# Performance work log

Measured on AMD Instinct MI355X. Metric: run time of the kernel, lower is better.

Reference implementation:

```python
import jax, jax.numpy as jnp
import numpy as np
from jax import lax

B, L, C_IN, D, H = 256, 4096, 2, 128, 4
DH = D // H          # 32 head dim
FF = 192             # round_up(1.3 * 128, 64)
NUM_CLASSES = 5
EPS = 1e-5


def setup_inputs() -> dict:
    key = jax.random.key(0)
    it = iter(jax.random.split(key, 48))
    def r(*s):
        return jax.random.normal(next(it), s, jnp.float32) * 0.1
    return dict(
        x=jax.random.normal(next(it), (B, L, C_IN), jnp.float32),
        w1a=r(16, C_IN, 4), w1b=r(16, C_IN, 2),
        bn1_g=jnp.ones((32,), jnp.float32), bn1_b=jnp.zeros((32,), jnp.float32),
        bn1_m=r(32), bn1_v=jnp.ones((32,), jnp.float32),
        w2=r(64, 32, 3),
        bn2_g=jnp.ones((64,), jnp.float32), bn2_b=jnp.zeros((64,), jnp.float32),
        bn2_m=r(64), bn2_v=jnp.ones((64,), jnp.float32),
        w3=r(D, 64, 3),
        bn3_g=jnp.ones((D,), jnp.float32), bn3_b=jnp.zeros((D,), jnp.float32),
        bn3_m=r(D), bn3_v=jnp.ones((D,), jnp.float32),
        ln1_w=jnp.ones((D,), jnp.float32),
        conv_w=r(D, 1, 3), conv_b=jnp.zeros((D,), jnp.float32),
        wi=r(H, DH, DH), wf=r(H, DH, DH), wz=r(H, DH, DH), wo=r(H, DH, DH),
        rkernel=r(H, DH, 4, DH), rbias=r(4, H, DH),
        gn_w=jnp.ones((D,), jnp.float32),
        ln2_w=jnp.ones((D,), jnp.float32),
        ffn_up_w=r(D, 2 * FF), ffn_down_w=r(FF, D),
        lnp_w=jnp.ones((D,), jnp.float32),
        fc_w=r(D, NUM_CLASSES), fc_b=jnp.zeros((NUM_CLASSES,), jnp.float32),
        lengths=jnp.full((B,), L, jnp.int32),
    )


def _leaky(x):
    return jnp.where(x >= 0, x, 0.01 * x)


def _bn(x, g, b, m, v):  # eval-mode batchnorm, x: (B, C, L)
    return (x - m[:, None]) * (g / jnp.sqrt(v + EPS))[:, None] + b[:, None]


def _conv(x, w, pad, groups=1):  # x: (B, C, L), w: (O, I/groups, K)
    return lax.conv_general_dilated(x, w, (1,), [pad],
                                    dimension_numbers=('NCH', 'OIH', 'NCH'),
                                    feature_group_count=groups)


def _pool(x):  # max pool kernel=2 stride=2 (floor)
    b, c, l = x.shape
    l2 = l // 2
    return x[:, :, :l2 * 2].reshape(b, c, l2, 2).max(-1)


def _ln(x, w):  # LayerNorm, weight only (xlstm lib default bias=False)
    mu = jnp.mean(x, -1, keepdims=True)
    var = jnp.mean((x - mu) ** 2, -1, keepdims=True)
    return (x - mu) * lax.rsqrt(var + EPS) * w


def _forward(x, w1a, w1b, bn1_g, bn1_b, bn1_m, bn1_v, w2, bn2_g, bn2_b, bn2_m, bn2_v,
             w3, bn3_g, bn3_b, bn3_m, bn3_v, ln1_w, conv_w, conv_b, wi, wf, wz, wo,
             rkernel, rbias, gn_w, ln2_w, ffn_up_w, ffn_down_w, lnp_w, fc_w, fc_b, lengths):
    b = x.shape[0]
    # ---- CNN stem (dropout = identity in eval) ----
    xc = jnp.transpose(x, (0, 2, 1))                      # (B, C_in, L)
    h = jnp.concatenate([_conv(xc, w1a, (1, 1)), _conv(xc, w1b, (0, 0))], 1)  # (B, 32, L-1)
    h = _pool(_leaky(_bn(h, bn1_g, bn1_b, bn1_m, bn1_v)))
    h = _pool(_leaky(_bn(_conv(h, w2, (0, 0)), bn2_g, bn2_b, bn2_m, bn2_v)))
    h = _pool(_leaky(_bn(_conv(h, w3, (0, 0)), bn3_g, bn3_b, bn3_m, bn3_v)))
    e = jnp.transpose(h, (0, 2, 1))                       # (B, S, D)
    s = e.shape[1]

    # ---- sLSTM block: pre-LN -> sLSTM layer -> residual ----
    xn = _ln(e, ln1_w)
    # causal depthwise conv (k=3, left pad 2) + SiLU, feeds i/f gates
    xcv = _conv(jnp.transpose(xn, (0, 2, 1)), conv_w, (2, 0), groups=D)
    xcv = jnp.transpose(jax.nn.silu(xcv + conv_b[:, None]), (0, 2, 1))  # (B, S, D)

    def hproj(t, w):  # headwise (block-diagonal) linear
        return jnp.einsum('bshd,hde->bshe', t.reshape(b, s, H, DH), w)

    gx = jnp.stack([hproj(xcv, wi), hproj(xcv, wf), hproj(xn, wz), hproj(xn, wo)], 2)
    gx = jnp.transpose(gx, (1, 0, 2, 3, 4)) + rbias       # (S, B, 4, H, DH)

    def step(carry, g):
        y, c, n, m = carry                                # each (B, H, DH)
        raw = g + jnp.einsum('bhd,hdge->bghe', y, rkernel)  # (B, 4, H, DH)
        iraw, fraw, zraw, oraw = raw[:, 0], raw[:, 1], raw[:, 2], raw[:, 3]
        logfplusm = m + jax.nn.log_sigmoid(fraw)
        mnew = jnp.maximum(iraw, logfplusm)               # stabilizer
        ig = jnp.exp(iraw - mnew)
        fg = jnp.exp(logfplusm - mnew)
        cnew = fg * c + ig * jnp.tanh(zraw)
        nnew = fg * n + ig
        ynew = jax.nn.sigmoid(oraw) * cnew / nnew
        return (ynew, cnew, nnew, mnew), ynew

    z0 = jnp.zeros((b, H, DH), e.dtype)
    _, ys = lax.scan(step, (z0, z0, z0, z0), gx)          # ys: (S, B, H, DH)
    y = jnp.transpose(ys, (1, 0, 2, 3))                   # (B, S, H, DH)
    mu = jnp.mean(y, -1, keepdims=True)
    var = jnp.mean((y - mu) ** 2, -1, keepdims=True)
    y = ((y - mu) * lax.rsqrt(var + EPS)).reshape(b, s, D) * gn_w  # per-head groupnorm
    e = e + y

    # ---- gated GELU feedforward -> residual ----
    xn2 = _ln(e, ln2_w)
    up = xn2 @ ffn_up_w                                   # (B, S, 2*FF)
    e = e + (jax.nn.gelu(up[..., :FF], approximate=False) * up[..., FF:]) @ ffn_down_w

    # ---- post-stack norm, last token, classifier head ----
    e = _ln(e, lnp_w)
    return e[:, -1, :] @ fc_w + fc_b                      # (B, NUM_CLASSES)


def reference(x, w1a, w1b, bn1_g, bn1_b, bn1_m, bn1_v, w2, bn2_g, bn2_b, bn2_m, bn2_v,
              w3, bn3_g, bn3_b, bn3_m, bn3_v, ln1_w, conv_w, conv_b, wi, wf, wz, wo,
              rkernel, rbias, gn_w, ln2_w, ffn_up_w, ffn_down_w, lnp_w, fc_w, fc_b, lengths):
    return _forward(x, w1a, w1b, bn1_g, bn1_b, bn1_m, bn1_v, w2, bn2_g, bn2_b, bn2_m, bn2_v,
                    w3, bn3_g, bn3_b, bn3_m, bn3_v, ln1_w, conv_w, conv_b, wi, wf, wz, wo,
                    rkernel, rbias, gn_w, ln2_w, ffn_up_w, ffn_down_w, lnp_w, fc_w, fc_b, lengths)
```

## Files before the change

kernel.cpp:

```cpp
#include <hip/hip_runtime.h>
#include <hip/hip_bf16.h>
#include <math.h>

#define EPS 1e-5f

typedef __attribute__((ext_vector_type(8))) _Float16 half8;
typedef __attribute__((ext_vector_type(4))) float f32x4;

static __device__ __forceinline__ unsigned short f16u(float x) {
  _Float16 h = (_Float16)x;
  return *(unsigned short*)&h;
}
static __device__ __forceinline__ float uf16(unsigned short u) {
  _Float16 h = *(_Float16*)&u;
  return (float)h;
}

__global__ __launch_bounds__(256) void kWTB2(const float* __restrict__ w2,
    const float* __restrict__ w3, unsigned short* __restrict__ o2,
    unsigned short* __restrict__ o3) {
  int idx = blockIdx.x * 256 + threadIdx.x;
  if (idx < 64 * 104) {
    int oc = idx / 104, kp = idx % 104;
    float v = 0.f;
    if (kp < 96) { int k = kp >> 5, ci = kp & 31; v = w2[oc * 96 + ci * 3 + k]; }
    o2[idx] = f16u(v);
  } else {
    int j = idx - 64 * 104;
    if (j < 128 * 200) {
      int oc = j / 200, kp = j % 200;
      float v = 0.f;
      if (kp < 192) { int k = kp >> 6, ci = kp & 63; v = w3[oc * 192 + ci * 3 + k]; }
      o3[j] = f16u(v);
    }
  }
}

__global__ __launch_bounds__(512) void kConv12(const float* __restrict__ x,
    const float* __restrict__ w1a, const float* __restrict__ w1b,
    const float* __restrict__ g1, const float* __restrict__ b1,
    const float* __restrict__ m1, const float* __restrict__ v1,
    const unsigned short* __restrict__ Bw, const float* __restrict__ g2,
    const float* __restrict__ b2, const float* __restrict__ m2,
    const float* __restrict__ v2, unsigned short* __restrict__ out2) {
  __shared__ _Float16 sA[130 * 40];
  __shared__ _Float16 sB[64 * 104];
  int tid = threadIdx.x;
  int b = blockIdx.z;
  int p0 = blockIdx.x * 128;
  {
    const unsigned int* src = (const unsigned int*)Bw;
    unsigned int* dst = (unsigned int*)sB;
    for (int i = tid; i < 64 * 104 / 2; i += 512) dst[i] = src[i];
  }
  {
    int c = tid & 31, rg = tid >> 5;
    float sc1 = g1[c] * rsqrtf(v1[c] + EPS);
    float sh1 = b1[c] - m1[c] * sc1;
    float wk0[4], wk1[4];
    if (c < 16) {
#pragma unroll
      for (int k = 0; k < 4; k++) { wk0[k] = w1a[c * 8 + k]; wk1[k] = w1a[c * 8 + 4 + k]; }
    } else {
      int cc = c - 16;
#pragma unroll
      for (int k = 0; k < 2; k++) { wk0[k] = w1b[cc * 4 + k]; wk1[k] = w1b[cc * 4 + 2 + k]; }
      wk0[2] = wk0[3] = wk1[2] = wk1[3] = 0.f;
    }
    const float2* xp = (const float2*)(x + (size_t)b * 8192);
    for (int r = rg; r < 130; r += 16) {
      int rr = p0 + r;
      _Float16 outv = (_Float16)0.f;
      if (rr < 2047) {
        float xv0[5], xv1[5];
#pragma unroll
        for (int j = 0; j < 5; j++) {
          int l = 2 * rr - 1 + j;
          if (l >= 0 && l < 4096) { float2 v = xp[l]; xv0[j] = v.x; xv1[j] = v.y; }
          else { xv0[j] = 0.f; xv1[j] = 0.f; }
        }
        float a0 = 0.f, a1 = 0.f;
        if (c < 16) {
#pragma unroll
          for (int k = 0; k < 4; k++) {
            a0 += xv0[k] * wk0[k] + xv1[k] * wk1[k];
            a1 += xv0[k + 1] * wk0[k] + xv1[k + 1] * wk1[k];
          }
        } else {
#pragma unroll
          for (int k = 0; k < 2; k++) {
            a0 += xv0[k + 1] * wk0[k] + xv1[k + 1] * wk1[k];
            a1 += xv0[k + 2] * wk0[k] + xv1[k + 2] * wk1[k];
          }
        }
        a0 = a0 * sc1 + sh1; a1 = a1 * sc1 + sh1;
        a0 = a0 >= 0.f ? a0 : 0.01f * a0;
        a1 = a1 >= 0.f ? a1 : 0.01f * a1;
        outv = (_Float16)fmaxf(a0, a1);
      }
      sA[r * 40 + c] = outv;
    }
  }
  __syncthreads();
  int lane = tid & 63, w = tid >> 6;
  int nrow = lane & 15, quad = lane >> 4;
  f32x4 acc[4];
#pragma unroll
  for (int i = 0; i < 4; i++) acc[i] = (f32x4){0.f, 0.f, 0.f, 0.f};
  int mbase = w * 16;
#pragma unroll
  for (int kk = 0; kk < 3; kk++) {
    half8 a = *(const half8*)(sA + (mbase + nrow + kk) * 40 + quad * 8);
#pragma unroll
    for (int ot = 0; ot < 4; ot++) {
      half8 bb = *(const half8*)(sB + (ot * 16 + nrow) * 104 + kk * 32 + quad * 8);
      acc[ot] = __builtin_amdgcn_mfma_f32_16x16x32_f16(a, bb, acc[ot], 0, 0, 0);
    }
  }
  int gm0 = p0 + mbase + quad * 4;
#pragma unroll
  for (int ot = 0; ot < 4; ot++) {
    int oc = ot * 16 + nrow;
    float sc = g2[oc] * rsqrtf(v2[oc] + EPS);
    float sh = b2[oc] - m2[oc] * sc;
    float v0 = acc[ot][0] * sc + sh, vv1 = acc[ot][1] * sc + sh;
    float v2e = acc[ot][2] * sc + sh, v3 = acc[ot][3] * sc + sh;
    v0 = v0 >= 0.f ? v0 : 0.01f * v0;
    vv1 = vv1 >= 0.f ? vv1 : 0.01f * vv1;
    v2e = v2e >= 0.f ? v2e : 0.01f * v2e;
    v3 = v3 >= 0.f ? v3 : 0.01f * v3;
    float pA = fmaxf(v0, vv1), pB = fmaxf(v2e, v3);
    int t0 = gm0 >> 1, t1 = t0 + 1;
    if (t0 < 1022) out2[((size_t)b * 1022 + t0) * 64 + oc] = f16u(pA);
    if (t1 < 1022) out2[((size_t)b * 1022 + t1) * 64 + oc] = f16u(pB);
  }
}

__global__ __launch_bounds__(512) void kConv3LN(const unsigned short* __restrict__ in,
    const unsigned short* __restrict__ Bw, const float* __restrict__ g,
    const float* __restrict__ bta, const float* __restrict__ mn,
    const float* __restrict__ vr, const float* __restrict__ lnw,
    unsigned short* __restrict__ xn, float* __restrict__ elast) {
  constexpr int IC = 64, OC = 128, LIN = 1022, AP = 72, BP = 200, KSTEPS = 6, OCT = 8;
  __shared__ _Float16 sA[130 * AP];
  __shared__ _Float16 sB[OC * BP];
  int tid = threadIdx.x;
  int b = blockIdx.z;
  int p0 = blockIdx.x * 128;
  {
    const unsigned int* src = (const unsigned int*)Bw;
    unsigned int* dst = (unsigned int*)sB;
    for (int i = tid; i < OC * BP / 2; i += 512) dst[i] = src[i];
  }
  {
    int q = tid % 8;
    for (int r = tid / 8; r < 130; r += 64) {
      int gp = p0 + r;
      uint4 val = {0u, 0u, 0u, 0u};
      if (gp < LIN) val = *(const uint4*)(in + ((size_t)b * LIN + gp) * IC + q * 8);
      *(uint4*)(sA + r * AP + q * 8) = val;
    }
  }
  __syncthreads();
  int lane = tid & 63, w = tid >> 6;
  int nrow = lane & 15, quad = lane >> 4;
  f32x4 acc[OCT];
#pragma unroll
  for (int i = 0; i < OCT; i++) acc[i] = (f32x4){0.f, 0.f, 0.f, 0.f};
  int mbase = w * 16;
#pragma unroll
  for (int kk = 0; kk < KSTEPS; kk++) {
    int k = kk >> 1;
    int ci0 = (kk & 1) * 32;
    half8 a = *(const half8*)(sA + (mbase + nrow + k) * AP + ci0 + quad * 8);
#pragma unroll
    for (int ot = 0; ot < OCT; ot++) {
      half8 bb = *(const half8*)(sB + (ot * 16 + nrow) * BP + kk * 32 + quad * 8);
      acc[ot] = __builtin_amdgcn_mfma_f32_16x16x32_f16(a, bb, acc[ot], 0, 0, 0);
    }
  }
  float pA[OCT], pB[OCT];
  float sA1 = 0.f, sA2 = 0.f, sB1 = 0.f, sB2 = 0.f;
#pragma unroll
  for (int ot = 0; ot < OCT; ot++) {
    int oc = ot * 16 + nrow;
    float sc = g[oc] * rsqrtf(vr[oc] + EPS);
    float sh = bta[oc] - mn[oc] * sc;
    float v0 = acc[ot][0] * sc + sh, v1 = acc[ot][1] * sc + sh;
    float v2 = acc[ot][2] * sc + sh, v3 = acc[ot][3] * sc + sh;
    v0 = v0 >= 0.f ? v0 : 0.01f * v0;
    v1 = v1 >= 0.f ? v1 : 0.01f * v1;
    v2 = v2 >= 0.f ? v2 : 0.01f * v2;
    v3 = v3 >= 0.f ? v3 : 0.01f * v3;
    float a = fmaxf(v0, v1), bb2 = fmaxf(v2, v3);
    pA[ot] = a; pB[ot] = bb2;
    sA1 += a; sA2 += a * a; sB1 += bb2; sB2 += bb2 * bb2;
  }
#pragma unroll
  for (int m = 1; m <= 8; m <<= 1) {
    sA1 += __shfl_xor(sA1, m); sA2 += __shfl_xor(sA2, m);
    sB1 += __shfl_xor(sB1, m); sB2 += __shfl_xor(sB2, m);
  }
  float muA = sA1 * (1.f / 128.f);
  float rsA = rsqrtf(sA2 * (1.f / 128.f) - muA * muA + EPS);
  float muB = sB1 * (1.f / 128.f);
  float rsB = rsqrtf(sB2 * (1.f / 128.f) - muB * muB + EPS);
  int t0 = (p0 + mbase + quad * 4) >> 1, t1 = t0 + 1;
#pragma unroll
  for (int ot = 0; ot < OCT; ot++) {
    int oc = ot * 16 + nrow;
    float lw = lnw[oc];
    if (t0 < 510) xn[((size_t)b * 510 + t0) * OC + oc] = f16u((pA[ot] - muA) * rsA * lw);
    if (t1 < 510) xn[((size_t)b * 510 + t1) * OC + oc] = f16u((pB[ot] - muB) * rsB * lw);
    if (t1 == 509) elast[b * 128 + oc] = pB[ot];
  }
}

__global__ __launch_bounds__(256) void kGxM(const unsigned short* __restrict__ xn,
    const float* __restrict__ cw, const float* __restrict__ cb,
    const float* __restrict__ wi, const float* __restrict__ wf,
    const float* __restrict__ wz, const float* __restrict__ wo,
    const float* __restrict__ rb, unsigned int* __restrict__ gx) {
  __shared__ __align__(16) char smem[29200];
  float* xnf = (float*)smem;
  _Float16* aX = (_Float16*)(smem + 8720);
  _Float16* aN = (_Float16*)(smem + 13840);
  unsigned short* ct = (unsigned short*)smem;
  _Float16* sW = (_Float16*)(smem + 18960);
  int bh = blockIdx.x, b = bh >> 2, h = bh & 3;
  int tid = threadIdx.x, lane = tid & 63, w = tid >> 6;
  int nrow = lane & 15, quad = lane >> 4;
  for (int idx = tid; idx < 4096; idx += 256) {
    int slot = idx >> 11, n = (idx >> 5) & 63, d = idx & 31;
    const float* wp = slot ? ((n >= 32) ? wo : wz) : ((n >= 32) ? wf : wi);
    sW[slot * 2560 + n * 40 + d] = (_Float16)wp[h * 1024 + d * 32 + (n & 31)];
  }
  int dd = tid & 31;
  float cw0 = cw[(h * 32 + dd) * 3], cw1 = cw[(h * 32 + dd) * 3 + 1],
        cw2 = cw[(h * 32 + dd) * 3 + 2], cbv = cb[h * 32 + dd];
  float bias0[4], bias1[4];
#pragma unroll
  for (int nt = 0; nt < 4; nt++) {
    int n = nt * 16 + nrow;
    bias0[nt] = rb[(n >> 5) * 128 + h * 32 + (n & 31)];
    bias1[nt] = rb[(2 + (n >> 5)) * 128 + h * 32 + (n & 31)];
  }
  __syncthreads();
  half8 bw0[4], bw1[4];
#pragma unroll
  for (int nt = 0; nt < 4; nt++) {
    bw0[nt] = *(const half8*)(sW + (nt * 16 + nrow) * 40 + quad * 8);
    bw1[nt] = *(const half8*)(sW + 2560 + (nt * 16 + nrow) * 40 + quad * 8);
  }
  const unsigned short* xb = xn + ((size_t)b * 510) * 128 + h * 32;
  for (int s0 = 0; s0 < 510; s0 += 64) {
    __syncthreads();
    {
      int d2 = tid & 15;
      for (int r = tid >> 4; r < 66; r += 16) {
        int s = s0 - 2 + r;
        unsigned int v = 0;
        if (s >= 0 && s < 510) v = *(const unsigned int*)(xb + (size_t)s * 128 + d2 * 2);
        xnf[r * 33 + d2 * 2]     = uf16(v & 0xFFFFu);
        xnf[r * 33 + d2 * 2 + 1] = uf16(v >> 16);
      }
    }
    __syncthreads();
    for (int m = tid >> 5; m < 64; m += 8) {
      float x0 = xnf[m * 33 + dd], x1 = xnf[(m + 1) * 33 + dd], x2 = xnf[(m + 2) * 33 + dd];
      float a = cbv + cw0 * x0 + cw1 * x1 + cw2 * x2;
      a = a * __builtin_amdgcn_rcpf(1.f + __expf(-a));
      aX[m * 40 + dd] = (_Float16)a;
      aN[m * 40 + dd] = (_Float16)x2;
    }
    __syncthreads();
    f32x4 z = (f32x4){0.f, 0.f, 0.f, 0.f};
    half8 ax = *(const half8*)(aX + (w * 16 + nrow) * 40 + quad * 8);
    half8 an = *(const half8*)(aN + (w * 16 + nrow) * 40 + quad * 8);
    f32x4 acc0[4], acc1[4];
#pragma unroll
    for (int nt = 0; nt < 4; nt++) {
      acc0[nt] = __builtin_amdgcn_mfma_f32_16x16x32_f16(ax, bw0[nt], z, 0, 0, 0);
      acc1[nt] = __builtin_amdgcn_mfma_f32_16x16x32_f16(an, bw1[nt], z, 0, 0, 0);
    }
    __syncthreads();
#pragma unroll
    for (int nt = 0; nt < 4; nt++) {
#pragma unroll
      for (int r = 0; r < 4; r++) {
        int row = w * 16 + quad * 4 + r;
        ct[row * 132 + 2 * (nt * 16 + nrow)]     = f16u(acc0[nt][r] + bias0[nt]);
        ct[row * 132 + 2 * (nt * 16 + nrow) + 1] = f16u(acc1[nt][r] + bias1[nt]);
      }
    }
    __syncthreads();
    {
      int u = tid & 63;
      for (int m = tid >> 6; m < 64; m += 4) {
        int s = s0 + m;
        if (s < 510)
          gx[((size_t)s * 1024 + bh) * 64 + u] = *(const unsigned int*)(ct + m * 132 + 2 * u);
      }
    }
  }
}

__global__ __launch_bounds__(64) void kRec(const unsigned int* __restrict__ gx,
    const float* __restrict__ rk, float* __restrict__ yf) {
  int bh = blockIdx.x; int h = bh & 3;
  int l = threadIdx.x; int half = l >> 5; int e = l & 31;
  float R1[32], R2[32];
  int g1 = half, g2 = 2 + half;
  const float* r1p = rk + h * 4096 + g1 * 32 + e;
  const float* r2p = rk + h * 4096 + g2 * 32 + e;
#pragma unroll
  for (int d = 0; d < 32; d++) { R1[d] = r1p[d * 128]; R2[d] = r2p[d * 128]; }
  const unsigned int* gp = gx + (size_t)bh * 64 + l;
  unsigned int buf[8];
#pragma unroll
  for (int j = 0; j < 8; j++) buf[j] = gp[(size_t)j * 65536];
  float y = 0.f, cst = 0.f, nst = 0.f, mst = 0.f;

  auto step = [&](unsigned int pc) {
    float a1 = uf16(pc & 0xFFFFu);
    float a2 = uf16(pc >> 16);
    float s10 = 0.f, s11 = 0.f, s12 = 0.f, s13 = 0.f;
    float s20 = 0.f, s21 = 0.f, s22 = 0.f, s23 = 0.f;
    unsigned int yb = __float_as_uint(y);
#pragma unroll
    for (int d = 0; d < 32; d += 4) {
      float y0 = __uint_as_float(__builtin_amdgcn_readlane(yb, d));
      float y1 = __uint_as_float(__builtin_amdgcn_readlane(yb, d + 1));
      float y2 = __uint_as_float(__builtin_amdgcn_readlane(yb, d + 2));
      float y3 = __uint_as_float(__builtin_amdgcn_readlane(yb, d + 3));
      s10 = fmaf(y0, R1[d], s10);     s20 = fmaf(y0, R2[d], s20);
      s11 = fmaf(y1, R1[d + 1], s11); s21 = fmaf(y1, R2[d + 1], s21);
      s12 = fmaf(y2, R1[d + 2], s12); s22 = fmaf(y2, R2[d + 2], s22);
      s13 = fmaf(y3, R1[d + 3], s13); s23 = fmaf(y3, R2[d + 3], s23);
    }
    a1 += (s10 + s11) + (s12 + s13);
    a2 += (s20 + s21) + (s22 + s23);
    float en = __expf(-fabsf(a1));
    float ls = fminf(a1, 0.f) - __logf(1.f + en);
    float sg = __builtin_amdgcn_rcpf(1.f + __expf(-a2));
    float tz = 1.f - 2.f * __builtin_amdgcn_rcpf(__expf(2.f * a2) + 1.f);
    float lsf = __shfl_xor(ls, 32);
    float so  = __shfl_xor(sg, 32);
    float lf = mst + lsf;
    float mnew = fmaxf(a1, lf);
    float ig = __expf(a1 - mnew);
    float fg = __expf(lf - mnew);
    cst = fg * cst + ig * tz;
    nst = fg * nst + ig;
    mst = mnew;
    y = so * cst * __builtin_amdgcn_rcpf(nst);
  };

  for (int s0 = 0; s0 < 504; s0 += 8) {
#pragma unroll
    for (int j = 0; j < 8; j++) {
      unsigned int pc = buf[j];
      int sn = s0 + j + 8; sn = sn > 509 ? 509 : sn;
      buf[j] = gp[(size_t)sn * 65536];
      step(pc);
    }
  }
#pragma unroll
  for (int j = 0; j < 6; j++) step(buf[j]);

  if (half == 0) yf[(bh >> 2) * 128 + h * 32 + e] = y;
}

__global__ __launch_bounds__(128) void kHead(const float* __restrict__ yf,
    const float* __restrict__ elast, const float* __restrict__ gnw,
    const float* __restrict__ ln2w, const float* __restrict__ upw,
    const float* __restrict__ dnw, const float* __restrict__ lnpw,
    const float* __restrict__ fcw, const float* __restrict__ fcb,
    float* __restrict__ outp) {
  int c = threadIdx.x; int b = blockIdx.x;
  __shared__ float sred[4];
  __shared__ float sx[128];
  __shared__ float sup[384];
  __shared__ float shh[192];
  float yv = yf[b * 128 + c];
  float s1 = yv, s2 = yv * yv;
#pragma unroll
  for (int m = 1; m <= 16; m <<= 1) { s1 += __shfl_xor(s1, m); s2 += __shfl_xor(s2, m); }
  float mu = s1 * (1.f / 32.f);
  float var = s2 * (1.f / 32.f) - mu * mu;
  float yn = (yv - mu) * rsqrtf(var + EPS) * gnw[c];
  float el = elast[b * 128 + c] + yn;
  auto ln128 = [&](float v, const float* w) -> float {
    float a = v, a2 = v * v;
#pragma unroll
    for (int m = 1; m <= 32; m <<= 1) { a += __shfl_xor(a, m); a2 += __shfl_xor(a2, m); }
    int wv = c >> 6;
    if ((c & 63) == 0) { sred[wv * 2] = a; sred[wv * 2 + 1] = a2; }
    __syncthreads();
    float t1 = sred[0] + sred[2], t2 = sred[1] + sred[3];
    __syncthreads();
    float mm = t1 * (1.f / 128.f);
    float vv = t2 * (1.f / 128.f) - mm * mm;
    return (v - mm) * rsqrtf(vv + EPS) * w[c];
  };
  float xn2 = ln128(el, ln2w);
  sx[c] = xn2;
  __syncthreads();
#pragma unroll
  for (int jj = 0; jj < 3; jj++) {
    int j = c + jj * 128;
    float acc = 0.f;
    for (int k = 0; k < 128; k++) acc += sx[k] * upw[k * 384 + j];
    sup[j] = acc;
  }
  __syncthreads();
  {
    float u = sup[c]; float mg = sup[192 + c];
    shh[c] = 0.5f * u * (1.f + erff(u * 0.70710678118654752f)) * mg;
    if (c < 64) {
      float u2 = sup[128 + c]; float m2 = sup[320 + c];
      shh[128 + c] = 0.5f * u2 * (1.f + erff(u2 * 0.70710678118654752f)) * m2;
    }
  }
  __syncthreads();
  float acc = 0.f;
  for (int f = 0; f < 192; f++) acc += shh[f] * dnw[f * 128 + c];
  float e2 = el + acc;
  float e3 = ln128(e2, lnpw);
  sx[c] = e3;
  __syncthreads();
  if (c < 5) {
    float a = fcb[c];
    for (int k = 0; k < 128; k++) a += sx[k] * fcw[k * 5 + c];
    outp[b * 5 + c] = a;
  }
}

extern "C" void kernel_launch(void* const* d_in, const int* in_sizes, int n_in,
                              void* d_out, int out_size, void* d_ws, size_t ws_size,
                              hipStream_t stream) {
  const float* x    = (const float*)d_in[0];
  const float* w1a  = (const float*)d_in[1];
  const float* w1b  = (const float*)d_in[2];
  const float* bn1g = (const float*)d_in[3];
  const float* bn1b = (const float*)d_in[4];
  const float* bn1m = (const float*)d_in[5];
  const float* bn1v = (const float*)d_in[6];
  const float* w2   = (const float*)d_in[7];
  const float* bn2g = (const float*)d_in[8];
  const float* bn2b = (const float*)d_in[9];
  const float* bn2m = (const float*)d_in[10];
  const float* bn2v = (const float*)d_in[11];
  const float* w3   = (const float*)d_in[12];
  const float* bn3g = (const float*)d_in[13];
  const float* bn3b = (const float*)d_in[14];
  const float* bn3m = (const float*)d_in[15];
  const float* bn3v = (const float*)d_in[16];
  const float* ln1w = (const float*)d_in[17];
  const float* cw   = (const float*)d_in[18];
  const float* cb   = (const float*)d_in[19];
  const float* wi   = (const float*)d_in[20];
  const float* wf   = (const float*)d_in[21];
  const float* wz   = (const float*)d_in[22];
  const float* wo   = (const float*)d_in[23];
  const float* rk   = (const float*)d_in[24];
  const float* rb   = (const float*)d_in[25];
  const float* gnw  = (const float*)d_in[26];
  const float* ln2w = (const float*)d_in[27];
  const float* upw  = (const float*)d_in[28];
  const float* dnw  = (const float*)d_in[29];
  const float* lnpw = (const float*)d_in[30];
  const float* fcw  = (const float*)d_in[31];
  const float* fcb  = (const float*)d_in[32];
  float* outp = (float*)d_out;

  char* ws = (char*)d_ws;
  unsigned short* xnb  = (unsigned short*)ws;
  unsigned short* out2 = (unsigned short*)(ws + ((size_t)34 << 20));
  unsigned int*   gxu  = (unsigned int*)(ws + ((size_t)34 << 20));
  float* elast = (float*)(ws + ((size_t)162 << 20));
  float* yfin  = (float*)(ws + ((size_t)163 << 20));
  unsigned short* wtg2 = (unsigned short*)(ws + ((size_t)164 << 20));
  unsigned short* wtg3 = (unsigned short*)(ws + ((size_t)164 << 20) + (64 << 10));

  kWTB2<<<dim3(126), 256, 0, stream>>>(w2, w3, wtg2, wtg3);
  kConv12<<<dim3(16, 1, 256), 512, 0, stream>>>(
      x, w1a, w1b, bn1g, bn1b, bn1m, bn1v, wtg2, bn2g, bn2b, bn2m, bn2v, out2);
  kConv3LN<<<dim3(8, 1, 256), 512, 0, stream>>>(
      out2, wtg3, bn3g, bn3b, bn3m, bn3v, ln1w, xnb, elast);
  kGxM<<<dim3(1024), 256, 0, stream>>>(xnb, cw, cb, wi, wf, wz, wo, rb, gxu);
  kRec<<<dim3(1024), 64, 0, stream>>>(gxu, rk, yfin);
  kHead<<<dim3(256), 128, 0, stream>>>(yfin, elast, gnw, ln2w, upw, dnw, lnpw, fcw, fcb, outp);
}
```

Measured before the change: 553.0 us.

## Store input-gate preactivation in full fp32 and split recurrence into two chunks

The input-gate preactivation a1 is now kept at full fp32 precision: its high 16 bits go into the packed gx word and the low 16 bits into a separate gxlo buffer, where before it was stored as fp16. The gate projection and the recurrence are each split into two time chunks (steps 0-256 and 256-510), with the recurrent state written to and reloaded from a global buffer between them. This looks aimed mainly at accuracy of the exponential gating, and the chunking keeps the workspace footprint bounded. In exchange it adds global traffic for gxlo, two extra kernel launches and a state round trip, and it changes the kRec unroll to a templated form with __launch_bounds__(64, 1).

Measured after the change: 533.5 us. 1.04x faster.

```diff
diff --git a/kernel.cpp b/kernel.cpp
--- a/kernel.cpp
+++ b/kernel.cpp
@@ -220,13 +220,15 @@
     const float* __restrict__ cw, const float* __restrict__ cb,
     const float* __restrict__ wi, const float* __restrict__ wf,
     const float* __restrict__ wz, const float* __restrict__ wo,
-    const float* __restrict__ rb, unsigned int* __restrict__ gx) {
-  __shared__ __align__(16) char smem[29200];
+    const float* __restrict__ rb, unsigned int* __restrict__ gx,
+    unsigned short* __restrict__ gxlo, int sBeg, int sEnd) {
+  __shared__ __align__(16) char smem[37904];
   float* xnf = (float*)smem;
   _Float16* aX = (_Float16*)(smem + 8720);
   _Float16* aN = (_Float16*)(smem + 13840);
   unsigned short* ct = (unsigned short*)smem;
   _Float16* sW = (_Float16*)(smem + 18960);
+  unsigned short* ct2 = (unsigned short*)(smem + 29200);
   int bh = blockIdx.x, b = bh >> 2, h = bh & 3;
   int tid = threadIdx.x, lane = tid & 63, w = tid >> 6;
   int nrow = lane & 15, quad = lane >> 4;
@@ -253,7 +255,7 @@
     bw1[nt] = *(const half8*)(sW + 2560 + (nt * 16 + nrow) * 40 + quad * 8);
   }
   const unsigned short* xb = xn + ((size_t)b * 510) * 128 + h * 32;
-  for (int s0 = 0; s0 < 510; s0 += 64) {
+  for (int s0 = sBeg; s0 < sEnd; s0 += 64) {
     __syncthreads();
     {
       int d2 = tid & 15;
@@ -289,8 +291,12 @@
 #pragma unroll
       for (int r = 0; r < 4; r++) {
         int row = w * 16 + quad * 4 + r;
-        ct[row * 132 + 2 * (nt * 16 + nrow)]     = f16u(acc0[nt][r] + bias0[nt]);
-        ct[row * 132 + 2 * (nt * 16 + nrow) + 1] = f16u(acc1[nt][r] + bias1[nt]);
+        int n = nt * 16 + nrow;
+        float A1 = acc0[nt][r] + bias0[nt];
+        unsigned int ab = __float_as_uint(A1);
+        ct[row * 132 + 2 * n]     = (unsigned short)(ab >> 16);
+        ct[row * 132 + 2 * n + 1] = f16u(acc1[nt][r] + bias1[nt]);
+        ct2[row * 68 + n]         = (unsigned short)(ab & 0xFFFFu);
       }
     }
     __syncthreads();
@@ -298,15 +304,20 @@
       int u = tid & 63;
       for (int m = tid >> 6; m < 64; m += 4) {
         int s = s0 + m;
-        if (s < 510)
-          gx[((size_t)s * 1024 + bh) * 64 + u] = *(const unsigned int*)(ct + m * 132 + 2 * u);
+        if (s < sEnd) {
+          size_t ri = ((size_t)(s - sBeg) * 1024 + bh) * 64 + u;
+          gx[ri]   = *(const unsigned int*)(ct + m * 132 + 2 * u);
+          gxlo[ri] = ct2[m * 68 + u];
+        }
       }
     }
   }
 }
 
-__global__ __launch_bounds__(64) void kRec(const unsigned int* __restrict__ gx,
-    const float* __restrict__ rk, float* __restrict__ yf) {
+template <int NS, bool FIRST, bool LAST>
+__global__ __launch_bounds__(64, 1) void kRecT(const unsigned int* __restrict__ gx,
+    const unsigned short* __restrict__ gxlo,
+    const float* __restrict__ rk, float* __restrict__ st, float* __restrict__ yf) {
   int bh = blockIdx.x; int h = bh & 3;
   int l = threadIdx.x; int half = l >> 5; int e = l & 31;
   float R1[32], R2[32];
@@ -316,14 +327,22 @@
 #pragma unroll
   for (int d = 0; d < 32; d++) { R1[d] = r1p[d * 128]; R2[d] = r2p[d * 128]; }
   const unsigned int* gp = gx + (size_t)bh * 64 + l;
+  const unsigned short* glp = gxlo + (size_t)bh * 64 + l;
   unsigned int buf[8];
-#pragma unroll
-  for (int j = 0; j < 8; j++) buf[j] = gp[(size_t)j * 65536];
-  float y = 0.f, cst = 0.f, nst = 0.f, mst = 0.f;
-
-  auto step = [&](unsigned int pc) {
-    float a1 = uf16(pc & 0xFFFFu);
-    float a2 = uf16(pc >> 16);
+  unsigned short bl[8];
+#pragma unroll
+  for (int j = 0; j < 8; j++) { buf[j] = gp[(size_t)j * 65536]; bl[j] = glp[(size_t)j * 65536]; }
+  int sidx = bh * 64 + l;
+  float y, cst, nst, mst;
+  if (FIRST) {
+    y = 0.f; cst = 0.f; nst = 0.f; mst = 0.f;
+  } else {
+    y = st[sidx]; cst = st[65536 + sidx]; nst = st[131072 + sidx]; mst = st[196608 + sidx];
+  }
+
+  auto step = [&](unsigned int pc, unsigned short lo) {
+    float a1 = __uint_as_float((pc << 16) | (unsigned int)lo);
+    float a2 = uf16((unsigned short)(pc >> 16));
     float s10 = 0.f, s11 = 0.f, s12 = 0.f, s13 = 0.f;
     float s20 = 0.f, s21 = 0.f, s22 = 0.f, s23 = 0.f;
     unsigned int yb = __float_as_uint(y);
@@ -356,19 +375,32 @@
     y = so * cst * __builtin_amdgcn_rcpf(nst);
   };
 
-  for (int s0 = 0; s0 < 504; s0 += 8) {
+  constexpr int NSF = NS & ~7;
+  for (int s0 = 0; s0 < NSF - 8; s0 += 8) {
 #pragma unroll
     for (int j = 0; j < 8; j++) {
-      unsigned int pc = buf[j];
-      int sn = s0 + j + 8; sn = sn > 509 ? 509 : sn;
-      buf[j] = gp[(size_t)sn * 65536];
-      step(pc);
-    }
-  }
-#pragma unroll
-  for (int j = 0; j < 6; j++) step(buf[j]);
-
-  if (half == 0) yf[(bh >> 2) * 128 + h * 32 + e] = y;
+      unsigned int pc = buf[j]; unsigned short lo = bl[j];
+      buf[j] = gp[(size_t)(s0 + j + 8) * 65536];
+      bl[j]  = glp[(size_t)(s0 + j + 8) * 65536];
+      step(pc, lo);
+    }
+  }
+#pragma unroll
+  for (int j = 0; j < 8; j++) {
+    unsigned int pc = buf[j]; unsigned short lo = bl[j];
+    int sn = NSF + j; sn = sn > NS - 1 ? NS - 1 : sn;
+    buf[j] = gp[(size_t)sn * 65536];
+    bl[j]  = glp[(size_t)sn * 65536];
+    step(pc, lo);
+  }
+#pragma unroll
+  for (int j = 0; j < NS - NSF; j++) step(buf[j], bl[j]);
+
+  if (LAST) {
+    if (half == 0) yf[(bh >> 2) * 128 + h * 32 + e] = y;
+  } else {
+    st[sidx] = y; st[65536 + sidx] = cst; st[131072 + sidx] = nst; st[196608 + sidx] = mst;
+  }
 }
 
 __global__ __launch_bounds__(128) void kHead(const float* __restrict__ yf,
@@ -478,17 +510,21 @@
   unsigned short* xnb  = (unsigned short*)ws;
   unsigned short* out2 = (unsigned short*)(ws + ((size_t)34 << 20));
   unsigned int*   gxu  = (unsigned int*)(ws + ((size_t)34 << 20));
-  float* elast = (float*)(ws + ((size_t)162 << 20));
-  float* yfin  = (float*)(ws + ((size_t)163 << 20));
-  unsigned short* wtg2 = (unsigned short*)(ws + ((size_t)164 << 20));
-  unsigned short* wtg3 = (unsigned short*)(ws + ((size_t)164 << 20) + (64 << 10));
+  unsigned short* gxlo = (unsigned short*)(ws + ((size_t)98 << 20));
+  float* st    = (float*)(ws + ((size_t)130 << 20));
+  float* elast = (float*)(ws + ((size_t)131 << 20));
+  float* yfin  = (float*)(ws + ((size_t)132 << 20));
+  unsigned short* wtg2 = (unsigned short*)(ws + ((size_t)133 << 20));
+  unsigned short* wtg3 = (unsigned short*)(ws + ((size_t)133 << 20) + (64 << 10));
 
   kWTB2<<<dim3(126), 256, 0, stream>>>(w2, w3, wtg2, wtg3);
   kConv12<<<dim3(16, 1, 256), 512, 0, stream>>>(
       x, w1a, w1b, bn1g, bn1b, bn1m, bn1v, wtg2, bn2g, bn2b, bn2m, bn2v, out2);
   kConv3LN<<<dim3(8, 1, 256), 512, 0, stream>>>(
       out2, wtg3, bn3g, bn3b, bn3m, bn3v, ln1w, xnb, elast);
-  kGxM<<<dim3(1024), 256, 0, stream>>>(xnb, cw, cb, wi, wf, wz, wo, rb, gxu);
-  kRec<<<dim3(1024), 64, 0, stream>>>(gxu, rk, yfin);
+  kGxM<<<dim3(1024), 256, 0, stream>>>(xnb, cw, cb, wi, wf, wz, wo, rb, gxu, gxlo, 0, 256);
+  kRecT<256, true, false><<<dim3(1024), 64, 0, stream>>>(gxu, gxlo, rk, st, yfin);
+  kGxM<<<dim3(1024), 256, 0, stream>>>(xnb, cw, cb, wi, wf, wz, wo, rb, gxu, gxlo, 256, 510);
+  kRecT<254, false, true><<<dim3(1024), 64, 0, stream>>>(gxu, gxlo, rk, st, yfin);
   kHead<<<dim3(256), 128, 0, stream>>>(yfin, elast, gnw, ln2w, upw, dnw, lnpw, fcw, fcb, outp);
 }
```
